# Optimization experiments

Measured on AMD Instinct MI355X. Metric: run time of the kernel, lower is better.

Reference implementation:

```python
import jax, jax.numpy as jnp
import numpy as np

QMIN, QMAX = -128.0, 127.0  # signed int8


def fake_quant(x):
    """Per-tensor symmetric int8 fake-quant (quantize-dequantize), scale from abs-max stats."""
    s = jax.lax.stop_gradient(jnp.max(jnp.abs(x)) / QMAX + 1e-8)
    q = x / s
    # straight-through rounding (matches brevitas STE; no-op for fwd-only)
    q = q + jax.lax.stop_gradient(jnp.clip(jnp.round(q), QMIN, QMAX) - q)
    return q * s


def setup_inputs() -> dict:
    key = jax.random.key(0)
    k1, k2, k3, k4, k5 = jax.random.split(key, 5)
    B, C, L, K, NC = 32, 1024, 4096, 4, 10
    x = jax.random.normal(k1, (B, C, L), dtype=jnp.float32)
    conv_w = jax.random.normal(k2, (C, 1, K), dtype=jnp.float32) * (1.0 / np.sqrt(K))
    conv_b = jax.random.normal(k3, (C,), dtype=jnp.float32) * 0.01
    lin_w = jax.random.normal(k4, (NC, C), dtype=jnp.float32) * (1.0 / np.sqrt(C))
    lin_b = jax.random.normal(k5, (NC,), dtype=jnp.float32) * 0.01
    return {"x": x, "conv_w": conv_w, "conv_b": conv_b, "lin_w": lin_w, "lin_b": lin_b}


def reference(x, conv_w, conv_b, lin_w, lin_b):
    # x: [B, C, L]
    C = x.shape[1]
    K = conv_w.shape[-1]
    # input_quant
    h = fake_quant(x)
    # causal depthwise conv1d with int8-fake-quant weights (QuantConv1dDepthwise)
    wq = fake_quant(conv_w)  # [C, 1, K]
    h = jax.lax.conv_general_dilated(
        h, wq,
        window_strides=(1,),
        padding=[(K - 1, 0)],  # causal: left-pad only
        dimension_numbers=("NCH", "OIH", "NCH"),
        feature_group_count=C,
    ) + conv_b[None, :, None]
    # conv_quant
    h = fake_quant(h)
    # QuantSiLU + silu_quant
    h = fake_quant(h * jax.nn.sigmoid(h))
    h = fake_quant(h)
    # global average pool over length, squeeze
    h = jnp.mean(h, axis=-1)  # [B, C]
    # pre_classifier_quant
    h = fake_quant(h)
    # QuantLinear with int8-fake-quant weights + bias
    logits = h @ fake_quant(lin_w).T + lin_b  # [B, num_classes]
    return logits
```

## Files before the change

### kernel.cpp

```cpp
#include <hip/hip_runtime.h>
#include <cstdint>
#include <cstddef>


static constexpr int BB = 32, CC = 1024, LL = 4096, NCLS = 10;
static constexpr long long NTOT = 1LL * BB * CC * LL;
static constexpr int ROWS = BB * CC;
static constexpr int G1 = 8192, G2 = 8192, G3 = 8192, G5 = 2048;

static constexpr int OF_LUT2 = 8;
static constexpr int OF_ABSY = 264;
static constexpr int OF_POOL = 1024;
static constexpr int OF_BM0  = 40960;
static constexpr int OF_BM1  = 49152;
static constexpr int OF_BM2  = 57344;
static constexpr int OF_BM3  = 65536;
static constexpr size_t OFFQ = 67584ull * 4ull;

__device__ __forceinline__ float qlvl_mul(float x, float rs) {
  return fminf(fmaxf(rintf(x * rs), -128.f), 127.f);
}
__device__ __forceinline__ float qlvl_div(float x, float s) {
  return fminf(fmaxf(rintf(x / s), -128.f), 127.f);
}
__device__ __forceinline__ float fq_div(float x, float s) {
  return qlvl_div(x, s) * s;
}
__device__ __forceinline__ float wred_max(float m) {
#pragma unroll
  for (int o = 32; o; o >>= 1) m = fmaxf(m, __shfl_xor(m, o));
  return m;
}
__device__ __forceinline__ float wred_sum(float s) {
#pragma unroll
  for (int o = 32; o; o >>= 1) s += __shfl_xor(s, o);
  return s;
}

__global__ void small_k(const float* __restrict__ cw, const float* __restrict__ lw, float* __restrict__ wsf) {
  __shared__ float red[256];
  const float* p = blockIdx.x ? lw : cw;
  int n = blockIdx.x ? NCLS * CC : CC * 4;
  float m = 0.f;
  for (int i = threadIdx.x; i < n; i += 256) m = fmaxf(m, fabsf(p[i]));
  red[threadIdx.x] = m; __syncthreads();
  for (int s = 128; s; s >>= 1) { if (threadIdx.x < s) red[threadIdx.x] = fmaxf(red[threadIdx.x], red[threadIdx.x + s]); __syncthreads(); }
  if (!threadIdx.x) wsf[blockIdx.x ? 5 : 1] = red[0];
}

__global__ __launch_bounds__(256) void p1_k(const float* __restrict__ x, float* __restrict__ bm) {
  __shared__ float red4[4];
  const float4* p4 = (const float4*)x;
  long long n4 = NTOT / 4;
  float m = 0.f;
  long long i = (long long)blockIdx.x * 256 + threadIdx.x;
  long long stride = (long long)G1 * 256;
  for (; i < n4; i += stride) {
    float4 v = p4[i];
    m = fmaxf(m, fmaxf(fmaxf(fabsf(v.x), fabsf(v.y)), fmaxf(fabsf(v.z), fabsf(v.w))));
  }
  m = wred_max(m);
  if ((threadIdx.x & 63) == 0) red4[threadIdx.x >> 6] = m;
  __syncthreads();
  if (!threadIdx.x) bm[blockIdx.x] = fmaxf(fmaxf(red4[0], red4[1]), fmaxf(red4[2], red4[3]));
}

__global__ void fin_k(const float* __restrict__ src, int n, float* __restrict__ dst) {
  __shared__ float red[256];
  float m = 0.f;
  for (int i = threadIdx.x; i < n; i += 256) m = fmaxf(m, src[i]);
  red[threadIdx.x] = m; __syncthreads();
  for (int s = 128; s; s >>= 1) { if (threadIdx.x < s) red[threadIdx.x] = fmaxf(red[threadIdx.x], red[threadIdx.x + s]); __syncthreads(); }
  if (!threadIdx.x) *dst = red[0];
}

__global__ __launch_bounds__(256) void p2_k(const float* __restrict__ x, const float* __restrict__ cw,
    const float* __restrict__ cb, const float* __restrict__ wsf,
    signed char* __restrict__ qx, float* __restrict__ bm) {
  __shared__ float red4[4];
  int tid = threadIdx.x;
  float s_x = wsf[0] / 127.f + 1e-8f, rs_x = 1.f / s_x;
  float s_w = wsf[1] / 127.f + 1e-8f;
  float s_xw = s_x * s_w;
  float m = 0.f;
  for (int row = blockIdx.x; row < ROWS; row += G2) {
    int c = row & (CC - 1);
    float wl0 = qlvl_div(cw[c * 4 + 0], s_w), wl1 = qlvl_div(cw[c * 4 + 1], s_w);
    float wl2 = qlvl_div(cw[c * 4 + 2], s_w), wl3 = qlvl_div(cw[c * 4 + 3], s_w);
    float bc = cb[c];
    const float* xr = x + 1LL * row * LL;
    int t0 = tid * 16;
    float lv[19];
    if (t0 == 0) { lv[0] = 0.f; lv[1] = 0.f; lv[2] = 0.f; }
    else {
      float4 p = *(const float4*)(xr + t0 - 4);
      lv[0] = qlvl_mul(p.y, rs_x); lv[1] = qlvl_mul(p.z, rs_x); lv[2] = qlvl_mul(p.w, rs_x);
    }
#pragma unroll
    for (int jj = 0; jj < 4; ++jj) {
      float4 v = *(const float4*)(xr + t0 + 4 * jj);
      lv[3 + 4 * jj] = qlvl_mul(v.x, rs_x); lv[4 + 4 * jj] = qlvl_mul(v.y, rs_x);
      lv[5 + 4 * jj] = qlvl_mul(v.z, rs_x); lv[6 + 4 * jj] = qlvl_mul(v.w, rs_x);
    }
    union { int4 v; signed char ch[16]; } pk;
#pragma unroll
    for (int j = 0; j < 16; ++j) {
      pk.ch[j] = (signed char)(int)lv[3 + j];
      float sum = lv[j] * wl0 + lv[j + 1] * wl1 + lv[j + 2] * wl2 + lv[j + 3] * wl3;
      float h = fmaf(s_xw, sum, bc);
      m = fmaxf(m, fabsf(h));
    }
    if (qx) *(int4*)(qx + 1LL * row * LL + t0) = pk.v;
  }
  m = wred_max(m);
  if ((tid & 63) == 0) red4[tid >> 6] = m;
  __syncthreads();
  if (!tid) bm[blockIdx.x] = fmaxf(fmaxf(red4[0], red4[1]), fmaxf(red4[2], red4[3]));
}

__global__ void finA_k(const float* __restrict__ src, int n, float* __restrict__ wsf, float* __restrict__ absY) {
  __shared__ float red[256];
  float m = 0.f;
  for (int i = threadIdx.x; i < n; i += 256) m = fmaxf(m, src[i]);
  red[threadIdx.x] = m; __syncthreads();
  for (int s = 128; s; s >>= 1) { if (threadIdx.x < s) red[threadIdx.x] = fmaxf(red[threadIdx.x], red[threadIdx.x + s]); __syncthreads(); }
  if (!threadIdx.x) wsf[2] = red[0];
  float s_c = red[0] / 127.f + 1e-8f;
  float v = (float)((int)threadIdx.x - 128) * s_c;
  float y = v * (1.f / (1.f + expf(-v)));
  absY[threadIdx.x] = fabsf(y);
}

__global__ __launch_bounds__(256) void p3_k(const signed char* __restrict__ qx, const float* __restrict__ cw,
    const float* __restrict__ cb, const float* __restrict__ wsf, const float* __restrict__ absY,
    signed char* __restrict__ qc, float* __restrict__ bm) {
  __shared__ float lutR[256 * 32];
  __shared__ float red4[4];
  int tid = threadIdx.x, t31 = tid & 31;
#pragma unroll
  for (int k = 0; k < 32; ++k) lutR[tid * 32 + k] = absY[tid];
  __syncthreads();
  float s_x = wsf[0] / 127.f + 1e-8f;
  float s_w = wsf[1] / 127.f + 1e-8f;
  float s_c = wsf[2] / 127.f + 1e-8f;
  float rs_c = 1.f / s_c, s_xw = s_x * s_w;
  float m = 0.f;
  for (int row = blockIdx.x; row < ROWS; row += G3) {
    int c = row & (CC - 1);
    float wl0 = qlvl_div(cw[c * 4 + 0], s_w), wl1 = qlvl_div(cw[c * 4 + 1], s_w);
    float wl2 = qlvl_div(cw[c * 4 + 2], s_w), wl3 = qlvl_div(cw[c * 4 + 3], s_w);
    float bc = cb[c];
    const signed char* qr = qx + 1LL * row * LL;
    int t0 = tid * 16;
    float lv[19];
    if (t0 == 0) { lv[0] = 0.f; lv[1] = 0.f; lv[2] = 0.f; }
    else {
      int pv = *(const int*)(qr + t0 - 4);
      lv[0] = (float)((signed char)(pv >> 8));
      lv[1] = (float)((signed char)(pv >> 16));
      lv[2] = (float)(pv >> 24);
    }
    union { int4 v; signed char ch[16]; } in;
    in.v = *(const int4*)(qr + t0);
#pragma unroll
    for (int j = 0; j < 16; ++j) lv[3 + j] = (float)in.ch[j];
    union { int4 v; signed char ch[16]; } out;
#pragma unroll
    for (int j = 0; j < 16; ++j) {
      float sum = lv[j] * wl0 + lv[j + 1] * wl1 + lv[j + 2] * wl2 + lv[j + 3] * wl3;
      float h = fmaf(s_xw, sum, bc);
      float qf = fminf(fmaxf(rintf(h * rs_c), -128.f), 127.f);
      out.ch[j] = (signed char)(int)qf;
      m = fmaxf(m, lutR[((int)qf + 128) * 32 + t31]);
    }
    *(int4*)(qc + 1LL * row * LL + t0) = out.v;
  }
  m = wred_max(m);
  if ((tid & 63) == 0) red4[tid >> 6] = m;
  __syncthreads();
  if (!tid) bm[blockIdx.x] = fmaxf(fmaxf(red4[0], red4[1]), fmaxf(red4[2], red4[3]));
}

__global__ __launch_bounds__(256) void p3b_k(const float* __restrict__ x, const float* __restrict__ cw,
    const float* __restrict__ cb, const float* __restrict__ wsf, const float* __restrict__ absY,
    signed char* __restrict__ qc, float* __restrict__ bm) {
  __shared__ float lutR[256 * 32];
  __shared__ float red4[4];
  int tid = threadIdx.x, t31 = tid & 31;
#pragma unroll
  for (int k = 0; k < 32; ++k) lutR[tid * 32 + k] = absY[tid];
  __syncthreads();
  float s_x = wsf[0] / 127.f + 1e-8f, rs_x = 1.f / s_x;
  float s_w = wsf[1] / 127.f + 1e-8f;
  float s_c = wsf[2] / 127.f + 1e-8f;
  float rs_c = 1.f / s_c, s_xw = s_x * s_w;
  float m = 0.f;
  for (int row = blockIdx.x; row < ROWS; row += G3) {
    int c = row & (CC - 1);
    float wl0 = qlvl_div(cw[c * 4 + 0], s_w), wl1 = qlvl_div(cw[c * 4 + 1], s_w);
    float wl2 = qlvl_div(cw[c * 4 + 2], s_w), wl3 = qlvl_div(cw[c * 4 + 3], s_w);
    float bc = cb[c];
    const float* xr = x + 1LL * row * LL;
    int t0 = tid * 16;
    float lv[19];
    if (t0 == 0) { lv[0] = 0.f; lv[1] = 0.f; lv[2] = 0.f; }
    else {
      float4 p = *(const float4*)(xr + t0 - 4);
      lv[0] = qlvl_mul(p.y, rs_x); lv[1] = qlvl_mul(p.z, rs_x); lv[2] = qlvl_mul(p.w, rs_x);
    }
#pragma unroll
    for (int jj = 0; jj < 4; ++jj) {
      float4 v = *(const float4*)(xr + t0 + 4 * jj);
      lv[3 + 4 * jj] = qlvl_mul(v.x, rs_x); lv[4 + 4 * jj] = qlvl_mul(v.y, rs_x);
      lv[5 + 4 * jj] = qlvl_mul(v.z, rs_x); lv[6 + 4 * jj] = qlvl_mul(v.w, rs_x);
    }
    union { int4 v; signed char ch[16]; } out;
#pragma unroll
    for (int j = 0; j < 16; ++j) {
      float sum = lv[j] * wl0 + lv[j + 1] * wl1 + lv[j + 2] * wl2 + lv[j + 3] * wl3;
      float h = fmaf(s_xw, sum, bc);
      float qf = fminf(fmaxf(rintf(h * rs_c), -128.f), 127.f);
      out.ch[j] = (signed char)(int)qf;
      m = fmaxf(m, lutR[((int)qf + 128) * 32 + t31]);
    }
    *(int4*)(qc + 1LL * row * LL + t0) = out.v;
  }
  m = wred_max(m);
  if ((tid & 63) == 0) red4[tid >> 6] = m;
  __syncthreads();
  if (!tid) bm[blockIdx.x] = fmaxf(fmaxf(red4[0], red4[1]), fmaxf(red4[2], red4[3]));
}

__global__ void finL_k(const float* __restrict__ src, int n, float* __restrict__ wsf, float* __restrict__ lut2) {
  __shared__ float red[256];
  float m = 0.f;
  for (int i = threadIdx.x; i < n; i += 256) m = fmaxf(m, src[i]);
  red[threadIdx.x] = m; __syncthreads();
  for (int s = 128; s; s >>= 1) { if (threadIdx.x < s) red[threadIdx.x] = fmaxf(red[threadIdx.x], red[threadIdx.x + s]); __syncthreads(); }
  float amax_y = red[0];
  if (!threadIdx.x) wsf[3] = amax_y;
  float s_c = wsf[2] / 127.f + 1e-8f;
  float s1 = amax_y / 127.f + 1e-8f;
  float maxj = fminf(fmaxf(rintf(amax_y / s1), -128.f), 127.f);
  float s2 = (maxj * s1) / 127.f + 1e-8f;
  float v = (float)((int)threadIdx.x - 128) * s_c;
  float y = v * (1.f / (1.f + expf(-v)));
  float y1 = fq_div(y, s1);
  lut2[threadIdx.x] = fq_div(y1, s2);
}

__global__ __launch_bounds__(256) void p5_k(const signed char* __restrict__ qc, const float* __restrict__ lut2,
    float* __restrict__ pooled, float* __restrict__ bm) {
  __shared__ float lutR[256 * 32];
  __shared__ float red4[4];
  int tid = threadIdx.x, t31 = tid & 31, lane = tid & 63, wid = tid >> 6;
#pragma unroll
  for (int k = 0; k < 32; ++k) lutR[tid * 32 + k] = lut2[tid];
  __syncthreads();
  float pm = 0.f;
  for (int row = blockIdx.x * 4 + wid; row < ROWS; row += G5 * 4) {
    const signed char* qr = qc + 1LL * row * LL;
    float sum = 0.f;
#pragma unroll
    for (int p = 0; p < 4; ++p) {
      union { int4 v; signed char ch[16]; } pk;
      pk.v = *(const int4*)(qr + p * 1024 + lane * 16);
#pragma unroll
      for (int k = 0; k < 16; ++k) sum += lutR[((int)pk.ch[k] + 128) * 32 + t31];
    }
    sum = wred_sum(sum);
    if (lane == 0) {
      float pv = sum * (1.f / (float)LL);
      pooled[row] = pv;
      pm = fmaxf(pm, fabsf(pv));
    }
  }
  pm = wred_max(pm);
  if (lane == 0) red4[wid] = pm;
  __syncthreads();
  if (!tid) bm[blockIdx.x] = fmaxf(fmaxf(red4[0], red4[1]), fmaxf(red4[2], red4[3]));
}

__global__ __launch_bounds__(256) void head_k(const float* __restrict__ pooled, const float* __restrict__ lw,
    const float* __restrict__ lb, const float* __restrict__ wsf, float* __restrict__ out) {
  __shared__ float red[256];
  int b = blockIdx.x / NCLS, n = blockIdx.x % NCLS;
  float s_p = wsf[4] / 127.f + 1e-8f, s_l = wsf[5] / 127.f + 1e-8f;
  float sum = 0.f;
  for (int ci = threadIdx.x; ci < CC; ci += 256)
    sum += fq_div(pooled[b * CC + ci], s_p) * fq_div(lw[n * CC + ci], s_l);
  red[threadIdx.x] = sum; __syncthreads();
  for (int s = 128; s; s >>= 1) { if (threadIdx.x < s) red[threadIdx.x] += red[threadIdx.x + s]; __syncthreads(); }
  if (!threadIdx.x) out[b * NCLS + n] = red[0] + lb[n];
}

extern "C" void kernel_launch(void* const* d_in, const int* in_sizes, int n_in,
                              void* d_out, int out_size, void* d_ws, size_t ws_size,
                              hipStream_t stream) {
  const float* x  = (const float*)d_in[0];
  const float* cw = (const float*)d_in[1];
  const float* cb = (const float*)d_in[2];
  const float* lw = (const float*)d_in[3];
  const float* lb = (const float*)d_in[4];
  float* out = (float*)d_out;
  float* wsf = (float*)d_ws;
  float* lut2   = wsf + OF_LUT2;
  float* absY   = wsf + OF_ABSY;
  float* pooled = wsf + OF_POOL;
  float* bm0 = wsf + OF_BM0;
  float* bm1 = wsf + OF_BM1;
  float* bm2 = wsf + OF_BM2;
  float* bm3 = wsf + OF_BM3;

  bool haveQX = ws_size >= OFFQ + 2ull * (size_t)NTOT;
  signed char* qx = (signed char*)d_ws + OFFQ;
  signed char* qc = haveQX ? qx + NTOT : qx;

  hipLaunchKernelGGL(small_k, dim3(2), dim3(256), 0, stream, cw, lw, wsf);
  hipLaunchKernelGGL(p1_k, dim3(G1), dim3(256), 0, stream, x, bm0);
  hipLaunchKernelGGL(fin_k, dim3(1), dim3(256), 0, stream, bm0, G1, wsf + 0);
  hipLaunchKernelGGL(p2_k, dim3(G2), dim3(256), 0, stream, x, cw, cb, wsf,
                     haveQX ? qx : (signed char*)nullptr, bm1);
  hipLaunchKernelGGL(finA_k, dim3(1), dim3(256), 0, stream, bm1, G2, wsf, absY);
  if (haveQX) {
    hipLaunchKernelGGL(p3_k, dim3(G3), dim3(256), 0, stream, qx, cw, cb, wsf, absY, qc, bm2);
  } else {
    hipLaunchKernelGGL(p3b_k, dim3(G3), dim3(256), 0, stream, x, cw, cb, wsf, absY, qc, bm2);
  }
  hipLaunchKernelGGL(finL_k, dim3(1), dim3(256), 0, stream, bm2, G3, wsf, lut2);
  hipLaunchKernelGGL(p5_k, dim3(G5), dim3(256), 0, stream, qc, lut2, pooled, bm3);
  hipLaunchKernelGGL(fin_k, dim3(1), dim3(256), 0, stream, bm3, G5, wsf + 4);
  hipLaunchKernelGGL(head_k, dim3(BB * NCLS), dim3(256), 0, stream, pooled, lw, lb, wsf, out);
}
```

Measured before the change: 966.2 us.

## Fuse all stages into one persistent kernel with grid barriers and recompute

```diff
diff --git a/kernel.cpp b/kernel.cpp
--- a/kernel.cpp
+++ b/kernel.cpp
@@ -6,16 +6,15 @@
 static constexpr int BB = 32, CC = 1024, LL = 4096, NCLS = 10;
 static constexpr long long NTOT = 1LL * BB * CC * LL;
 static constexpr int ROWS = BB * CC;
-static constexpr int G1 = 8192, G2 = 8192, G3 = 8192, G5 = 2048;
-
-static constexpr int OF_LUT2 = 8;
-static constexpr int OF_ABSY = 264;
-static constexpr int OF_POOL = 1024;
-static constexpr int OF_BM0  = 40960;
-static constexpr int OF_BM1  = 49152;
-static constexpr int OF_BM2  = 57344;
-static constexpr int OF_BM3  = 65536;
-static constexpr size_t OFFQ = 67584ull * 4ull;
+static constexpr int NB = 1024;
+static_assert(NB == CC, "block==channel mapping requires NB==CC");
+
+static constexpr int OF_BM0 = 64;
+static constexpr int OF_BM1 = 1088;
+static constexpr int OF_BM2 = 2112;
+static constexpr int OF_BM3 = 3136;
+static constexpr int OF_POOL = 4160;
+static constexpr size_t OFFQ = 36928ull * 4ull;
 
 __device__ __forceinline__ float qlvl_mul(float x, float rs) {
   return fminf(fmaxf(rintf(x * rs), -128.f), 127.f);
@@ -26,272 +25,254 @@
 __device__ __forceinline__ float fq_div(float x, float s) {
   return qlvl_div(x, s) * s;
 }
-__device__ __forceinline__ float wred_max(float m) {
-#pragma unroll
-  for (int o = 32; o; o >>= 1) m = fmaxf(m, __shfl_xor(m, o));
-  return m;
-}
 __device__ __forceinline__ float wred_sum(float s) {
 #pragma unroll
   for (int o = 32; o; o >>= 1) s += __shfl_xor(s, o);
   return s;
 }
 
-__global__ void small_k(const float* __restrict__ cw, const float* __restrict__ lw, float* __restrict__ wsf) {
-  __shared__ float red[256];
-  const float* p = blockIdx.x ? lw : cw;
-  int n = blockIdx.x ? NCLS * CC : CC * 4;
-  float m = 0.f;
-  for (int i = threadIdx.x; i < n; i += 256) m = fmaxf(m, fabsf(p[i]));
-  red[threadIdx.x] = m; __syncthreads();
-  for (int s = 128; s; s >>= 1) { if (threadIdx.x < s) red[threadIdx.x] = fmaxf(red[threadIdx.x], red[threadIdx.x + s]); __syncthreads(); }
-  if (!threadIdx.x) wsf[blockIdx.x ? 5 : 1] = red[0];
-}
-
-__global__ __launch_bounds__(256) void p1_k(const float* __restrict__ x, float* __restrict__ bm) {
-  __shared__ float red4[4];
-  const float4* p4 = (const float4*)x;
-  long long n4 = NTOT / 4;
-  float m = 0.f;
-  long long i = (long long)blockIdx.x * 256 + threadIdx.x;
-  long long stride = (long long)G1 * 256;
-  for (; i < n4; i += stride) {
-    float4 v = p4[i];
-    m = fmaxf(m, fmaxf(fmaxf(fabsf(v.x), fabsf(v.y)), fmaxf(fabsf(v.z), fabsf(v.w))));
-  }
-  m = wred_max(m);
-  if ((threadIdx.x & 63) == 0) red4[threadIdx.x >> 6] = m;
-  __syncthreads();
-  if (!threadIdx.x) bm[blockIdx.x] = fmaxf(fmaxf(red4[0], red4[1]), fmaxf(red4[2], red4[3]));
-}
-
-__global__ void fin_k(const float* __restrict__ src, int n, float* __restrict__ dst) {
-  __shared__ float red[256];
-  float m = 0.f;
-  for (int i = threadIdx.x; i < n; i += 256) m = fmaxf(m, src[i]);
-  red[threadIdx.x] = m; __syncthreads();
-  for (int s = 128; s; s >>= 1) { if (threadIdx.x < s) red[threadIdx.x] = fmaxf(red[threadIdx.x], red[threadIdx.x + s]); __syncthreads(); }
-  if (!threadIdx.x) *dst = red[0];
-}
-
-__global__ __launch_bounds__(256) void p2_k(const float* __restrict__ x, const float* __restrict__ cw,
-    const float* __restrict__ cb, const float* __restrict__ wsf,
-    signed char* __restrict__ qx, float* __restrict__ bm) {
-  __shared__ float red4[4];
-  int tid = threadIdx.x;
-  float s_x = wsf[0] / 127.f + 1e-8f, rs_x = 1.f / s_x;
-  float s_w = wsf[1] / 127.f + 1e-8f;
-  float s_xw = s_x * s_w;
-  float m = 0.f;
-  for (int row = blockIdx.x; row < ROWS; row += G2) {
-    int c = row & (CC - 1);
-    float wl0 = qlvl_div(cw[c * 4 + 0], s_w), wl1 = qlvl_div(cw[c * 4 + 1], s_w);
-    float wl2 = qlvl_div(cw[c * 4 + 2], s_w), wl3 = qlvl_div(cw[c * 4 + 3], s_w);
-    float bc = cb[c];
-    const float* xr = x + 1LL * row * LL;
-    int t0 = tid * 16;
-    float lv[19];
-    if (t0 == 0) { lv[0] = 0.f; lv[1] = 0.f; lv[2] = 0.f; }
-    else {
-      float4 p = *(const float4*)(xr + t0 - 4);
-      lv[0] = qlvl_mul(p.y, rs_x); lv[1] = qlvl_mul(p.z, rs_x); lv[2] = qlvl_mul(p.w, rs_x);
-    }
-#pragma unroll
-    for (int jj = 0; jj < 4; ++jj) {
-      float4 v = *(const float4*)(xr + t0 + 4 * jj);
-      lv[3 + 4 * jj] = qlvl_mul(v.x, rs_x); lv[4 + 4 * jj] = qlvl_mul(v.y, rs_x);
-      lv[5 + 4 * jj] = qlvl_mul(v.z, rs_x); lv[6 + 4 * jj] = qlvl_mul(v.w, rs_x);
-    }
-    union { int4 v; signed char ch[16]; } pk;
-#pragma unroll
-    for (int j = 0; j < 16; ++j) {
-      pk.ch[j] = (signed char)(int)lv[3 + j];
-      float sum = lv[j] * wl0 + lv[j + 1] * wl1 + lv[j + 2] * wl2 + lv[j + 3] * wl3;
-      float h = fmaf(s_xw, sum, bc);
-      m = fmaxf(m, fabsf(h));
-    }
-    if (qx) *(int4*)(qx + 1LL * row * LL + t0) = pk.v;
-  }
-  m = wred_max(m);
-  if ((tid & 63) == 0) red4[tid >> 6] = m;
-  __syncthreads();
-  if (!tid) bm[blockIdx.x] = fmaxf(fmaxf(red4[0], red4[1]), fmaxf(red4[2], red4[3]));
-}
-
-__global__ void finA_k(const float* __restrict__ src, int n, float* __restrict__ wsf, float* __restrict__ absY) {
-  __shared__ float red[256];
-  float m = 0.f;
-  for (int i = threadIdx.x; i < n; i += 256) m = fmaxf(m, src[i]);
-  red[threadIdx.x] = m; __syncthreads();
-  for (int s = 128; s; s >>= 1) { if (threadIdx.x < s) red[threadIdx.x] = fmaxf(red[threadIdx.x], red[threadIdx.x + s]); __syncthreads(); }
-  if (!threadIdx.x) wsf[2] = red[0];
-  float s_c = red[0] / 127.f + 1e-8f;
-  float v = (float)((int)threadIdx.x - 128) * s_c;
-  float y = v * (1.f / (1.f + expf(-v)));
-  absY[threadIdx.x] = fabsf(y);
-}
-
-__global__ __launch_bounds__(256) void p3_k(const signed char* __restrict__ qx, const float* __restrict__ cw,
-    const float* __restrict__ cb, const float* __restrict__ wsf, const float* __restrict__ absY,
-    signed char* __restrict__ qc, float* __restrict__ bm) {
+__device__ __forceinline__ float bred_max(float v, float* redS) {
+  int t = threadIdx.x;
+  redS[t] = v; __syncthreads();
+  for (int s = 128; s; s >>= 1) { if (t < s) redS[t] = fmaxf(redS[t], redS[t + s]); __syncthreads(); }
+  float r = redS[0]; __syncthreads();
+  return r;
+}
+
+__device__ __forceinline__ void gbar(unsigned* cnt, unsigned target) {
+  __syncthreads();
+  __threadfence();
+  if (threadIdx.x == 0) {
+    atomicAdd(cnt, 1u);
+    unsigned spins = 0;
+    while (__hip_atomic_load(cnt, __ATOMIC_RELAXED, __HIP_MEMORY_SCOPE_AGENT) < target) {
+      __builtin_amdgcn_s_sleep(16);
+      if (++spins > 20000000u) break;
+    }
+  }
+  __syncthreads();
+  __threadfence();
+}
+
+__global__ __launch_bounds__(256, 4) void mega_k(
+    const float* __restrict__ x, const float* __restrict__ cw, const float* __restrict__ cb,
+    const float* __restrict__ lw, const float* __restrict__ lb,
+    float* __restrict__ out, float* __restrict__ wsf, signed char* __restrict__ qx,
+    unsigned* __restrict__ cnt) {
   __shared__ float lutR[256 * 32];
-  __shared__ float red4[4];
-  int tid = threadIdx.x, t31 = tid & 31;
-#pragma unroll
-  for (int k = 0; k < 32; ++k) lutR[tid * 32 + k] = absY[tid];
-  __syncthreads();
-  float s_x = wsf[0] / 127.f + 1e-8f;
-  float s_w = wsf[1] / 127.f + 1e-8f;
-  float s_c = wsf[2] / 127.f + 1e-8f;
-  float rs_c = 1.f / s_c, s_xw = s_x * s_w;
-  float m = 0.f;
-  for (int row = blockIdx.x; row < ROWS; row += G3) {
-    int c = row & (CC - 1);
-    float wl0 = qlvl_div(cw[c * 4 + 0], s_w), wl1 = qlvl_div(cw[c * 4 + 1], s_w);
-    float wl2 = qlvl_div(cw[c * 4 + 2], s_w), wl3 = qlvl_div(cw[c * 4 + 3], s_w);
-    float bc = cb[c];
-    const signed char* qr = qx + 1LL * row * LL;
-    int t0 = tid * 16;
-    float lv[19];
-    if (t0 == 0) { lv[0] = 0.f; lv[1] = 0.f; lv[2] = 0.f; }
-    else {
-      int pv = *(const int*)(qr + t0 - 4);
-      lv[0] = (float)((signed char)(pv >> 8));
-      lv[1] = (float)((signed char)(pv >> 16));
-      lv[2] = (float)(pv >> 24);
-    }
-    union { int4 v; signed char ch[16]; } in;
-    in.v = *(const int4*)(qr + t0);
-#pragma unroll
-    for (int j = 0; j < 16; ++j) lv[3 + j] = (float)in.ch[j];
-    union { int4 v; signed char ch[16]; } out;
-#pragma unroll
-    for (int j = 0; j < 16; ++j) {
-      float sum = lv[j] * wl0 + lv[j + 1] * wl1 + lv[j + 2] * wl2 + lv[j + 3] * wl3;
-      float h = fmaf(s_xw, sum, bc);
-      float qf = fminf(fmaxf(rintf(h * rs_c), -128.f), 127.f);
-      out.ch[j] = (signed char)(int)qf;
-      m = fmaxf(m, lutR[((int)qf + 128) * 32 + t31]);
-    }
-    *(int4*)(qc + 1LL * row * LL + t0) = out.v;
-  }
-  m = wred_max(m);
-  if ((tid & 63) == 0) red4[tid >> 6] = m;
-  __syncthreads();
-  if (!tid) bm[blockIdx.x] = fmaxf(fmaxf(red4[0], red4[1]), fmaxf(red4[2], red4[3]));
-}
-
-__global__ __launch_bounds__(256) void p3b_k(const float* __restrict__ x, const float* __restrict__ cw,
-    const float* __restrict__ cb, const float* __restrict__ wsf, const float* __restrict__ absY,
-    signed char* __restrict__ qc, float* __restrict__ bm) {
-  __shared__ float lutR[256 * 32];
-  __shared__ float red4[4];
-  int tid = threadIdx.x, t31 = tid & 31;
-#pragma unroll
-  for (int k = 0; k < 32; ++k) lutR[tid * 32 + k] = absY[tid];
-  __syncthreads();
-  float s_x = wsf[0] / 127.f + 1e-8f, rs_x = 1.f / s_x;
-  float s_w = wsf[1] / 127.f + 1e-8f;
-  float s_c = wsf[2] / 127.f + 1e-8f;
-  float rs_c = 1.f / s_c, s_xw = s_x * s_w;
-  float m = 0.f;
-  for (int row = blockIdx.x; row < ROWS; row += G3) {
-    int c = row & (CC - 1);
-    float wl0 = qlvl_div(cw[c * 4 + 0], s_w), wl1 = qlvl_div(cw[c * 4 + 1], s_w);
-    float wl2 = qlvl_div(cw[c * 4 + 2], s_w), wl3 = qlvl_div(cw[c * 4 + 3], s_w);
-    float bc = cb[c];
-    const float* xr = x + 1LL * row * LL;
-    int t0 = tid * 16;
-    float lv[19];
-    if (t0 == 0) { lv[0] = 0.f; lv[1] = 0.f; lv[2] = 0.f; }
-    else {
-      float4 p = *(const float4*)(xr + t0 - 4);
-      lv[0] = qlvl_mul(p.y, rs_x); lv[1] = qlvl_mul(p.z, rs_x); lv[2] = qlvl_mul(p.w, rs_x);
-    }
-#pragma unroll
-    for (int jj = 0; jj < 4; ++jj) {
-      float4 v = *(const float4*)(xr + t0 + 4 * jj);
-      lv[3 + 4 * jj] = qlvl_mul(v.x, rs_x); lv[4 + 4 * jj] = qlvl_mul(v.y, rs_x);
-      lv[5 + 4 * jj] = qlvl_mul(v.z, rs_x); lv[6 + 4 * jj] = qlvl_mul(v.w, rs_x);
-    }
-    union { int4 v; signed char ch[16]; } out;
-#pragma unroll
-    for (int j = 0; j < 16; ++j) {
-      float sum = lv[j] * wl0 + lv[j + 1] * wl1 + lv[j + 2] * wl2 + lv[j + 3] * wl3;
-      float h = fmaf(s_xw, sum, bc);
-      float qf = fminf(fmaxf(rintf(h * rs_c), -128.f), 127.f);
-      out.ch[j] = (signed char)(int)qf;
-      m = fmaxf(m, lutR[((int)qf + 128) * 32 + t31]);
-    }
-    *(int4*)(qc + 1LL * row * LL + t0) = out.v;
-  }
-  m = wred_max(m);
-  if ((tid & 63) == 0) red4[tid >> 6] = m;
-  __syncthreads();
-  if (!tid) bm[blockIdx.x] = fmaxf(fmaxf(red4[0], red4[1]), fmaxf(red4[2], red4[3]));
-}
-
-__global__ void finL_k(const float* __restrict__ src, int n, float* __restrict__ wsf, float* __restrict__ lut2) {
-  __shared__ float red[256];
-  float m = 0.f;
-  for (int i = threadIdx.x; i < n; i += 256) m = fmaxf(m, src[i]);
-  red[threadIdx.x] = m; __syncthreads();
-  for (int s = 128; s; s >>= 1) { if (threadIdx.x < s) red[threadIdx.x] = fmaxf(red[threadIdx.x], red[threadIdx.x + s]); __syncthreads(); }
-  float amax_y = red[0];
-  if (!threadIdx.x) wsf[3] = amax_y;
-  float s_c = wsf[2] / 127.f + 1e-8f;
-  float s1 = amax_y / 127.f + 1e-8f;
-  float maxj = fminf(fmaxf(rintf(amax_y / s1), -128.f), 127.f);
-  float s2 = (maxj * s1) / 127.f + 1e-8f;
-  float v = (float)((int)threadIdx.x - 128) * s_c;
-  float y = v * (1.f / (1.f + expf(-v)));
-  float y1 = fq_div(y, s1);
-  lut2[threadIdx.x] = fq_div(y1, s2);
-}
-
-__global__ __launch_bounds__(256) void p5_k(const signed char* __restrict__ qc, const float* __restrict__ lut2,
-    float* __restrict__ pooled, float* __restrict__ bm) {
-  __shared__ float lutR[256 * 32];
-  __shared__ float red4[4];
-  int tid = threadIdx.x, t31 = tid & 31, lane = tid & 63, wid = tid >> 6;
-#pragma unroll
-  for (int k = 0; k < 32; ++k) lutR[tid * 32 + k] = lut2[tid];
-  __syncthreads();
-  float pm = 0.f;
-  for (int row = blockIdx.x * 4 + wid; row < ROWS; row += G5 * 4) {
-    const signed char* qr = qc + 1LL * row * LL;
+  __shared__ float redS[256];
+  const int tid = threadIdx.x, blk = blockIdx.x;
+  const int t31 = tid & 31, lane = tid & 63, wid = tid >> 6;
+
+  float acw = 0.f;
+#pragma unroll
+  for (int i = 0; i < 16; ++i) acw = fmaxf(acw, fabsf(cw[tid + 256 * i]));
+  acw = bred_max(acw, redS);
+  float alw = 0.f;
+  for (int i = tid; i < NCLS * CC; i += 256) alw = fmaxf(alw, fabsf(lw[i]));
+  alw = bred_max(alw, redS);
+  const float s_w = acw / 127.f + 1e-8f;
+  const float s_l = alw / 127.f + 1e-8f;
+
+  {
+    const float4* p4 = (const float4*)x;
+    float m = 0.f;
+    const long long n4 = NTOT / 4, stride = (long long)NB * 256;
+    for (long long i = (long long)blk * 256 + tid; i < n4; i += stride) {
+      float4 v = p4[i];
+      m = fmaxf(m, fmaxf(fmaxf(fabsf(v.x), fabsf(v.y)), fmaxf(fabsf(v.z), fabsf(v.w))));
+    }
+    m = bred_max(m, redS);
+    if (!tid) wsf[OF_BM0 + blk] = m;
+  }
+  gbar(cnt, 1u * NB);
+  float m = fmaxf(fmaxf(wsf[OF_BM0 + tid], wsf[OF_BM0 + tid + 256]),
+                  fmaxf(wsf[OF_BM0 + tid + 512], wsf[OF_BM0 + tid + 768]));
+  const float amax_x = bred_max(m, redS);
+  const float s_x = amax_x / 127.f + 1e-8f, rs_x = 1.f / s_x;
+  const float s_xw = s_x * s_w;
+
+  const int c = blk;
+  const float wl0 = qlvl_div(cw[c * 4 + 0], s_w), wl1 = qlvl_div(cw[c * 4 + 1], s_w);
+  const float wl2 = qlvl_div(cw[c * 4 + 2], s_w), wl3 = qlvl_div(cw[c * 4 + 3], s_w);
+  const float bc = cb[c];
+
+  {
+    float mH = 0.f;
+    const int t0 = tid * 16;
+    for (int k = 0; k < BB; ++k) {
+      const int row = blk + (k << 10);
+      const float* xr = x + 1LL * row * LL;
+      float lv[19];
+      if (t0 == 0) { lv[0] = 0.f; lv[1] = 0.f; lv[2] = 0.f; }
+      else {
+        float4 p = *(const float4*)(xr + t0 - 4);
+        lv[0] = qlvl_mul(p.y, rs_x); lv[1] = qlvl_mul(p.z, rs_x); lv[2] = qlvl_mul(p.w, rs_x);
+      }
+#pragma unroll
+      for (int jj = 0; jj < 4; ++jj) {
+        float4 v = *(const float4*)(xr + t0 + 4 * jj);
+        lv[3 + 4 * jj] = qlvl_mul(v.x, rs_x); lv[4 + 4 * jj] = qlvl_mul(v.y, rs_x);
+        lv[5 + 4 * jj] = qlvl_mul(v.z, rs_x); lv[6 + 4 * jj] = qlvl_mul(v.w, rs_x);
+      }
+      union { int4 v; signed char ch[16]; } pk;
+#pragma unroll
+      for (int j = 0; j < 16; ++j) {
+        pk.ch[j] = (signed char)(int)lv[3 + j];
+        float sum = lv[j] * wl0 + lv[j + 1] * wl1 + lv[j + 2] * wl2 + lv[j + 3] * wl3;
+        float h = fmaf(s_xw, sum, bc);
+        mH = fmaxf(mH, fabsf(h));
+      }
+      if (qx) *(int4*)(qx + 1LL * row * LL + t0) = pk.v;
+    }
+    mH = bred_max(mH, redS);
+    if (!tid) wsf[OF_BM1 + blk] = mH;
+  }
+  gbar(cnt, 2u * NB);
+  m = fmaxf(fmaxf(wsf[OF_BM1 + tid], wsf[OF_BM1 + tid + 256]),
+            fmaxf(wsf[OF_BM1 + tid + 512], wsf[OF_BM1 + tid + 768]));
+  const float amax_h = bred_max(m, redS);
+  const float s_c = amax_h / 127.f + 1e-8f, rs_c = 1.f / s_c;
+
+  {
+    float v = (float)(tid - 128) * s_c;
+    float y = v * (1.f / (1.f + expf(-v)));
+    float ay = fabsf(y);
+#pragma unroll
+    for (int r = 0; r < 32; ++r) lutR[tid * 32 + r] = ay;
+  }
+  __syncthreads();
+
+  {
+    float mS = 0.f;
+    const int t0 = tid * 16;
+    for (int k = 0; k < BB; ++k) {
+      const int row = blk + (k << 10);
+      float lv[19];
+      if (qx) {
+        const signed char* qr = qx + 1LL * row * LL;
+        if (t0 == 0) { lv[0] = 0.f; lv[1] = 0.f; lv[2] = 0.f; }
+        else {
+          int pv = *(const int*)(qr + t0 - 4);
+          lv[0] = (float)((signed char)(pv >> 8));
+          lv[1] = (float)((signed char)(pv >> 16));
+          lv[2] = (float)(pv >> 24);
+        }
+        union { int4 v; signed char ch[16]; } in; in.v = *(const int4*)(qr + t0);
+#pragma unroll
+        for (int j = 0; j < 16; ++j) lv[3 + j] = (float)in.ch[j];
+      } else {
+        const float* xr = x + 1LL * row * LL;
+        if (t0 == 0) { lv[0] = 0.f; lv[1] = 0.f; lv[2] = 0.f; }
+        else {
+          float4 p = *(const float4*)(xr + t0 - 4);
+          lv[0] = qlvl_mul(p.y, rs_x); lv[1] = qlvl_mul(p.z, rs_x); lv[2] = qlvl_mul(p.w, rs_x);
+        }
+#pragma unroll
+        for (int jj = 0; jj < 4; ++jj) {
+          float4 v = *(const float4*)(xr + t0 + 4 * jj);
+          lv[3 + 4 * jj] = qlvl_mul(v.x, rs_x); lv[4 + 4 * jj] = qlvl_mul(v.y, rs_x);
+          lv[5 + 4 * jj] = qlvl_mul(v.z, rs_x); lv[6 + 4 * jj] = qlvl_mul(v.w, rs_x);
+        }
+      }
+#pragma unroll
+      for (int j = 0; j < 16; ++j) {
+        float sum = lv[j] * wl0 + lv[j + 1] * wl1 + lv[j + 2] * wl2 + lv[j + 3] * wl3;
+        float h = fmaf(s_xw, sum, bc);
+        float qf = fminf(fmaxf(rintf(h * rs_c), -128.f), 127.f);
+        mS = fmaxf(mS, lutR[((int)qf + 128) * 32 + t31]);
+      }
+    }
+    mS = bred_max(mS, redS);
+    if (!tid) wsf[OF_BM2 + blk] = mS;
+  }
+  gbar(cnt, 3u * NB);
+  m = fmaxf(fmaxf(wsf[OF_BM2 + tid], wsf[OF_BM2 + tid + 256]),
+            fmaxf(wsf[OF_BM2 + tid + 512], wsf[OF_BM2 + tid + 768]));
+  const float amax_y = bred_max(m, redS);
+
+  {
+    float s1 = amax_y / 127.f + 1e-8f;
+    float maxj = fminf(fmaxf(rintf(amax_y / s1), -128.f), 127.f);
+    float s2 = (maxj * s1) / 127.f + 1e-8f;
+    float v = (float)(tid - 128) * s_c;
+    float y = v * (1.f / (1.f + expf(-v)));
+    float y1 = fq_div(y, s1);
+    float l2v = fq_div(y1, s2);
+    __syncthreads();
+#pragma unroll
+    for (int r = 0; r < 32; ++r) lutR[tid * 32 + r] = l2v;
+  }
+  __syncthreads();
+
+  {
+    float pm = 0.f;
+    for (int k = 0; k < 8; ++k) {
+      const int row = blk + ((wid + 4 * k) << 10);
+      const signed char* qr = qx ? qx + 1LL * row * LL : nullptr;
+      const float* xr = x + 1LL * row * LL;
+      float sum = 0.f;
+#pragma unroll
+      for (int p = 0; p < 4; ++p) {
+        const int t0 = p * 1024 + lane * 16;
+        float lv[19];
+        if (qx) {
+          if (t0 == 0) { lv[0] = 0.f; lv[1] = 0.f; lv[2] = 0.f; }
+          else {
+            int pv = *(const int*)(qr + t0 - 4);
+            lv[0] = (float)((signed char)(pv >> 8));
+            lv[1] = (float)((signed char)(pv >> 16));
+            lv[2] = (float)(pv >> 24);
+          }
+          union { int4 v; signed char ch[16]; } in; in.v = *(const int4*)(qr + t0);
+#pragma unroll
+          for (int j = 0; j < 16; ++j) lv[3 + j] = (float)in.ch[j];
+        } else {
+          if (t0 == 0) { lv[0] = 0.f; lv[1] = 0.f; lv[2] = 0.f; }
+          else {
+            float4 pp = *(const float4*)(xr + t0 - 4);
+            lv[0] = qlvl_mul(pp.y, rs_x); lv[1] = qlvl_mul(pp.z, rs_x); lv[2] = qlvl_mul(pp.w, rs_x);
+          }
+#pragma unroll
+          for (int jj = 0; jj < 4; ++jj) {
+            float4 v = *(const float4*)(xr + t0 + 4 * jj);
+            lv[3 + 4 * jj] = qlvl_mul(v.x, rs_x); lv[4 + 4 * jj] = qlvl_mul(v.y, rs_x);
+            lv[5 + 4 * jj] = qlvl_mul(v.z, rs_x); lv[6 + 4 * jj] = qlvl_mul(v.w, rs_x);
+          }
+        }
+#pragma unroll
+        for (int j = 0; j < 16; ++j) {
+          float s4 = lv[j] * wl0 + lv[j + 1] * wl1 + lv[j + 2] * wl2 + lv[j + 3] * wl3;
+          float h = fmaf(s_xw, s4, bc);
+          float qf = fminf(fmaxf(rintf(h * rs_c), -128.f), 127.f);
+          sum += lutR[((int)qf + 128) * 32 + t31];
+        }
+      }
+      sum = wred_sum(sum);
+      if (lane == 0) {
+        float pv = sum * (1.f / (float)LL);
+        wsf[OF_POOL + row] = pv;
+        pm = fmaxf(pm, fabsf(pv));
+      }
+    }
+    pm = bred_max(pm, redS);
+    if (!tid) wsf[OF_BM3 + blk] = pm;
+  }
+  gbar(cnt, 4u * NB);
+  m = fmaxf(fmaxf(wsf[OF_BM3 + tid], wsf[OF_BM3 + tid + 256]),
+            fmaxf(wsf[OF_BM3 + tid + 512], wsf[OF_BM3 + tid + 768]));
+  const float aP = bred_max(m, redS);
+
+  if (blk < BB * NCLS) {
+    const float s_p = aP / 127.f + 1e-8f;
+    const int b = blk / NCLS, n = blk - b * NCLS;
     float sum = 0.f;
-#pragma unroll
-    for (int p = 0; p < 4; ++p) {
-      union { int4 v; signed char ch[16]; } pk;
-      pk.v = *(const int4*)(qr + p * 1024 + lane * 16);
-#pragma unroll
-      for (int k = 0; k < 16; ++k) sum += lutR[((int)pk.ch[k] + 128) * 32 + t31];
-    }
-    sum = wred_sum(sum);
-    if (lane == 0) {
-      float pv = sum * (1.f / (float)LL);
-      pooled[row] = pv;
-      pm = fmaxf(pm, fabsf(pv));
-    }
-  }
-  pm = wred_max(pm);
-  if (lane == 0) red4[wid] = pm;
-  __syncthreads();
-  if (!tid) bm[blockIdx.x] = fmaxf(fmaxf(red4[0], red4[1]), fmaxf(red4[2], red4[3]));
-}
-
-__global__ __launch_bounds__(256) void head_k(const float* __restrict__ pooled, const float* __restrict__ lw,
-    const float* __restrict__ lb, const float* __restrict__ wsf, float* __restrict__ out) {
-  __shared__ float red[256];
-  int b = blockIdx.x / NCLS, n = blockIdx.x % NCLS;
-  float s_p = wsf[4] / 127.f + 1e-8f, s_l = wsf[5] / 127.f + 1e-8f;
-  float sum = 0.f;
-  for (int ci = threadIdx.x; ci < CC; ci += 256)
-    sum += fq_div(pooled[b * CC + ci], s_p) * fq_div(lw[n * CC + ci], s_l);
-  red[threadIdx.x] = sum; __syncthreads();
-  for (int s = 128; s; s >>= 1) { if (threadIdx.x < s) red[threadIdx.x] += red[threadIdx.x + s]; __syncthreads(); }
-  if (!threadIdx.x) out[b * NCLS + n] = red[0] + lb[n];
+    for (int ci = tid; ci < CC; ci += 256)
+      sum += fq_div(wsf[OF_POOL + b * CC + ci], s_p) * fq_div(lw[n * CC + ci], s_l);
+    redS[tid] = sum; __syncthreads();
+    for (int s = 128; s; s >>= 1) { if (tid < s) redS[tid] += redS[tid + s]; __syncthreads(); }
+    if (!tid) out[b * NCLS + n] = redS[0] + lb[n];
+  }
 }
 
 extern "C" void kernel_launch(void* const* d_in, const int* in_sizes, int n_in,
@@ -302,33 +283,11 @@
   const float* cb = (const float*)d_in[2];
   const float* lw = (const float*)d_in[3];
   const float* lb = (const float*)d_in[4];
-  float* out = (float*)d_out;
   float* wsf = (float*)d_ws;
-  float* lut2   = wsf + OF_LUT2;
-  float* absY   = wsf + OF_ABSY;
-  float* pooled = wsf + OF_POOL;
-  float* bm0 = wsf + OF_BM0;
-  float* bm1 = wsf + OF_BM1;
-  float* bm2 = wsf + OF_BM2;
-  float* bm3 = wsf + OF_BM3;
-
-  bool haveQX = ws_size >= OFFQ + 2ull * (size_t)NTOT;
-  signed char* qx = (signed char*)d_ws + OFFQ;
-  signed char* qc = haveQX ? qx + NTOT : qx;
-
-  hipLaunchKernelGGL(small_k, dim3(2), dim3(256), 0, stream, cw, lw, wsf);
-  hipLaunchKernelGGL(p1_k, dim3(G1), dim3(256), 0, stream, x, bm0);
-  hipLaunchKernelGGL(fin_k, dim3(1), dim3(256), 0, stream, bm0, G1, wsf + 0);
-  hipLaunchKernelGGL(p2_k, dim3(G2), dim3(256), 0, stream, x, cw, cb, wsf,
-                     haveQX ? qx : (signed char*)nullptr, bm1);
-  hipLaunchKernelGGL(finA_k, dim3(1), dim3(256), 0, stream, bm1, G2, wsf, absY);
-  if (haveQX) {
-    hipLaunchKernelGGL(p3_k, dim3(G3), dim3(256), 0, stream, qx, cw, cb, wsf, absY, qc, bm2);
-  } else {
-    hipLaunchKernelGGL(p3b_k, dim3(G3), dim3(256), 0, stream, x, cw, cb, wsf, absY, qc, bm2);
-  }
-  hipLaunchKernelGGL(finL_k, dim3(1), dim3(256), 0, stream, bm2, G3, wsf, lut2);
-  hipLaunchKernelGGL(p5_k, dim3(G5), dim3(256), 0, stream, qc, lut2, pooled, bm3);
-  hipLaunchKernelGGL(fin_k, dim3(1), dim3(256), 0, stream, bm3, G5, wsf + 4);
-  hipLaunchKernelGGL(head_k, dim3(BB * NCLS), dim3(256), 0, stream, pooled, lw, lb, wsf, out);
-}
+  unsigned* cnt = (unsigned*)d_ws;
+  signed char* qx = (ws_size >= OFFQ + (size_t)NTOT) ? (signed char*)d_ws + OFFQ
+                                                     : (signed char*)nullptr;
+  hipMemsetAsync(d_ws, 0, 256, stream);
+  hipLaunchKernelGGL(mega_k, dim3(NB), dim3(256), 0, stream,
+                     x, cw, cb, lw, lb, (float*)d_out, wsf, qx, cnt);
+}
```

Result: slower. 1.829 ms (+89.3%).
